# Performance work log

Hardware: AMD Instinct MI355X
Metric: run time of the kernel (lower is better)

The kernel has to match this reference:

```python
import jax, jax.numpy as jnp
import numpy as np

B, C, H, W = 8, 32, 512, 512
WS = 8
CQ = C // 4                      # 8
N = (H // WS) * (W // WS)        # 4096 windows
ED = WS * WS * C                 # 2048 embed_dim
EPS = 1e-6


def setup_inputs() -> dict:
    key = jax.random.key(0)
    ks = jax.random.split(key, 16)
    s = 0.02
    return {
        "input_x": jax.random.normal(ks[0], (B, C, H, W), jnp.float32),
        # in_conv: Conv2d(C, C//4, 1)
        "w_in": jax.random.normal(ks[1], (CQ, C), jnp.float32) * s,
        "b_in": jnp.zeros((CQ,), jnp.float32),
        # conv: Conv2d(C, C//4, 1) + LayerNorm(C//4)
        "w_conv": jax.random.normal(ks[2], (CQ, C), jnp.float32) * s,
        "b_conv": jnp.zeros((CQ,), jnp.float32),
        "ln_w": jnp.ones((CQ,), jnp.float32),
        "ln_b": jnp.zeros((CQ,), jnp.float32),
        # out_CA: Conv2d(C//4, C, 1)
        "w_ca": jax.random.normal(ks[3], (C, CQ), jnp.float32) * s,
        "b_ca": jnp.zeros((C,), jnp.float32),
        # out_SA: Conv2d(C//4, 1, 3, pad 1)
        "w_sa": jax.random.normal(ks[4], (1, CQ, 3, 3), jnp.float32) * s,
        "b_sa": jnp.zeros((1,), jnp.float32),
        # out_mask MLP: Linear(ED, ED//2), Linear(ED//2, ED)  (torch weight [out,in])
        "w_m1": jax.random.normal(ks[5], (ED // 2, ED), jnp.float32) * s,
        "b_m1": jnp.zeros((ED // 2,), jnp.float32),
        "w_m2": jax.random.normal(ks[6], (ED, ED // 2), jnp.float32) * s,
        "b_m2": jnp.zeros((ED,), jnp.float32),
    }


def _leaky(x):
    return jax.nn.leaky_relu(x, 0.1)


def _conv1x1(x, w, b):
    # x: [B,Cin,H,W], w: [Cout,Cin]
    return jnp.einsum('bchw,oc->bohw', x, w) + b[None, :, None, None]


def reference(input_x, w_in, b_in, w_conv, b_conv, ln_w, ln_b,
              w_ca, b_ca, w_sa, b_sa, w_m1, b_m1, w_m2, b_m2):
    b_, c_, h_, w_ = input_x.shape
    n_win = (h_ // WS) * (w_ // WS)

    # in_conv branch
    x = _leaky(_conv1x1(input_x, w_in, b_in))          # [B,CQ,H,W]

    # conv branch: 1x1 conv -> channels_first LayerNorm -> leaky
    x_ = _conv1x1(input_x, w_conv, b_conv)             # [B,CQ,H,W]
    u = jnp.mean(x_, axis=1, keepdims=True)
    s = jnp.mean((x_ - u) ** 2, axis=1, keepdims=True)
    x_ = (x_ - u) / jnp.sqrt(s + EPS)
    x_ = _leaky(ln_w[None, :, None, None] * x_ + ln_b[None, :, None, None])

    # channel attention: global avg pool -> 1x1 conv -> sigmoid
    pooled = jnp.mean(x_, axis=(2, 3), keepdims=True)  # [B,CQ,1,1]
    ca = jax.nn.sigmoid(_conv1x1(pooled, w_ca, b_ca))  # [B,C,1,1]

    # spatial attention: 3x3 conv -> sigmoid
    sa = jax.lax.conv_general_dilated(
        x_, w_sa, (1, 1), 'SAME',
        dimension_numbers=('NCHW', 'OIHW', 'NCHW')) + b_sa[None, :, None, None]
    sa = jax.nn.sigmoid(sa)                            # [B,1,H,W]

    # window variance + bottom-k mask
    xm = jnp.mean(x, axis=1)                           # [B,H,W]
    xw = xm.reshape(b_, h_ // WS, WS, w_ // WS, WS)
    xw = xw.transpose(0, 1, 3, 2, 4).reshape(b_, n_win, WS * WS)  # [B,N,64]
    var_x = jnp.var(xw, axis=-1, ddof=1)               # [B,N] (torch unbiased var)
    k_top = n_win // 2
    _, idx = jax.lax.top_k(-var_x, k_top)              # indices of smallest-variance windows
    mask = jnp.ones((b_, n_win), input_x.dtype)
    mask = mask.at[jnp.arange(b_)[:, None], idx].set(0.0)  # vectorized scatter

    # broadcast 0/1 mask across embed dim, then MLP (see notes re: original bug)
    m = jnp.broadcast_to(mask[:, :, None], (b_, n_win, w_m1.shape[1]))
    hdd = _leaky(jnp.einsum('bnd,ed->bne', m, w_m1) + b_m1)
    out_mask = jnp.einsum('bne,fe->bnf', hdd, w_m2) + b_m2  # [B,N,ED]

    return (out_mask, ca, sa)
```

## Files before the change

kernel.cpp:

```cpp
#include <hip/hip_runtime.h>
#include <math.h>

#define B_   8
#define C_   32
#define H_   512
#define W_   512
#define CQ_  8
#define NW_  4096
#define ED_  2048
#define EH_  1024
#define EPS_ 1e-6f

#define AS1 __attribute__((address_space(1)))
#define AS3 __attribute__((address_space(3)))

__device__ __forceinline__ float leaky(float x) { return x > 0.f ? x : 0.1f * x; }
__device__ __forceinline__ float sigmoidf_(float x) { return 1.f / (1.f + __expf(-x)); }

__global__ __launch_bounds__(256) void pass_a(
    const float* __restrict__ x,
    const float* __restrict__ w_in, const float* __restrict__ b_in,
    const float* __restrict__ w_conv, const float* __restrict__ b_conv,
    const float* __restrict__ ln_w, const float* __restrict__ ln_b,
    float* __restrict__ xq_out,
    double* __restrict__ var_out,
    float* __restrict__ pooled_part)
{
    __shared__ float stage[4][6][256];
    __shared__ float red[4][CQ_];

    const int tid  = threadIdx.x;
    const int lane = tid & 63, wv = tid >> 6;
    const int sx   = blockIdx.x;
    const int band = blockIdx.y;
    const int b    = blockIdx.z;
    const size_t plane = (size_t)H_ * W_;
    const float* xb = x + (size_t)b * C_ * plane;

    const int row0 = band * 8 + (lane >> 3);
    const int col0 = sx * 128 + wv * 32 + (lane & 7) * 4;
    const float* gw = xb + (size_t)row0 * W_ + col0;

#define STAGE(slot, c)                                                         \
    __builtin_amdgcn_global_load_lds(                                          \
        (const AS1 unsigned int*)(gw + (size_t)(c) * plane),                   \
        (AS3 unsigned int*)(&stage[wv][slot][0]), 16, 0, 0);

    float ycv[CQ_][4], yin[CQ_][4];
#pragma unroll
    for (int q = 0; q < CQ_; ++q)
#pragma unroll
        for (int j = 0; j < 4; ++j) { ycv[q][j] = 0.f; yin[q][j] = 0.f; }

    STAGE(0, 0) STAGE(1, 1) STAGE(2, 2) STAGE(3, 3) STAGE(4, 4) STAGE(5, 5)

#pragma unroll
    for (int c = 0; c < C_; ++c) {
        if (c < 27)       asm volatile("s_waitcnt vmcnt(5)" ::: "memory");
        else if (c == 27) asm volatile("s_waitcnt vmcnt(4)" ::: "memory");
        else if (c == 28) asm volatile("s_waitcnt vmcnt(3)" ::: "memory");
        else if (c == 29) asm volatile("s_waitcnt vmcnt(2)" ::: "memory");
        else if (c == 30) asm volatile("s_waitcnt vmcnt(1)" ::: "memory");
        else              asm volatile("s_waitcnt vmcnt(0)" ::: "memory");

        const float4 v = *reinterpret_cast<const float4*>(&stage[wv][c % 6][lane * 4]);
#pragma unroll
        for (int q = 0; q < CQ_; ++q) {
            const float wc = w_conv[q * C_ + c];
            const float wi = w_in[q * C_ + c];
            ycv[q][0] = fmaf(wc, v.x, ycv[q][0]);
            ycv[q][1] = fmaf(wc, v.y, ycv[q][1]);
            ycv[q][2] = fmaf(wc, v.z, ycv[q][2]);
            ycv[q][3] = fmaf(wc, v.w, ycv[q][3]);
            yin[q][0] = fmaf(wi, v.x, yin[q][0]);
            yin[q][1] = fmaf(wi, v.y, yin[q][1]);
            yin[q][2] = fmaf(wi, v.z, yin[q][2]);
            yin[q][3] = fmaf(wi, v.w, yin[q][3]);
        }
        if (c + 6 < C_) {
            asm volatile("s_waitcnt lgkmcnt(0)" ::: "memory");
            STAGE(c % 6, c + 6)
        }
    }
#undef STAGE

#pragma unroll
    for (int q = 0; q < CQ_; ++q) {
        const float bc = b_conv[q];
#pragma unroll
        for (int j = 0; j < 4; ++j) ycv[q][j] += bc;
    }

    float ps[CQ_];
#pragma unroll
    for (int q = 0; q < CQ_; ++q) ps[q] = 0.f;

    float xmv[4];
#pragma unroll
    for (int j = 0; j < 4; ++j) {
        float u = 0.f;
#pragma unroll
        for (int q = 0; q < CQ_; ++q) u += ycv[q][j];
        u *= 0.125f;
        float s = 0.f;
#pragma unroll
        for (int q = 0; q < CQ_; ++q) { const float d = ycv[q][j] - u; s = fmaf(d, d, s); }
        s *= 0.125f;
        const float inv = 1.f / sqrtf(s + EPS_);
        float m = 0.f;
#pragma unroll
        for (int q = 0; q < CQ_; ++q) {
            const float xv = leaky(fmaf(ln_w[q], (ycv[q][j] - u) * inv, ln_b[q]));
            ycv[q][j] = xv;
            ps[q] += xv;
            m += leaky(yin[q][j] + b_in[q]);
        }
        xmv[j] = m * 0.125f;
    }

#pragma unroll
    for (int q = 0; q < CQ_; ++q) {
        *reinterpret_cast<float4*>(
            &xq_out[(((size_t)b * CQ_ + q) * H_ + row0) * W_ + col0]) =
            make_float4(ycv[q][0], ycv[q][1], ycv[q][2], ycv[q][3]);
    }

    {
        double s = (double)xmv[0] + (double)xmv[1] + (double)xmv[2] + (double)xmv[3];
        s += __shfl_xor(s, 1);
        s += __shfl_xor(s, 8);
        s += __shfl_xor(s, 16);
        s += __shfl_xor(s, 32);
        const double mean = s * (1.0 / 64.0);
        double s2 = 0.0;
#pragma unroll
        for (int j = 0; j < 4; ++j) {
            const double d = (double)xmv[j] - mean;
            s2 += d * d;
        }
        s2 += __shfl_xor(s2, 1);
        s2 += __shfl_xor(s2, 8);
        s2 += __shfl_xor(s2, 16);
        s2 += __shfl_xor(s2, 32);
        if ((lane >> 3) == 0 && (lane & 1) == 0) {
            const int k = (lane & 7) >> 1;
            const int n = band * 64 + sx * 16 + wv * 4 + k;
            var_out[(size_t)b * NW_ + n] = s2 * (1.0 / 63.0);
        }
    }

#pragma unroll
    for (int q = 0; q < CQ_; ++q) {
        float s = ps[q];
#pragma unroll
        for (int off = 32; off; off >>= 1) s += __shfl_xor(s, off);
        if (lane == 0) red[wv][q] = s;
    }
    __syncthreads();
    if (tid < CQ_) {
        const float s = red[0][tid] + red[1][tid] + red[2][tid] + red[3][tid];
        const int bid = ((int)blockIdx.z * 64 + blockIdx.y) * 4 + blockIdx.x;
        pooled_part[bid * CQ_ + tid] = s;
    }
}

__global__ __launch_bounds__(256) void sa_kernel(
    const float* __restrict__ xq,
    const float* __restrict__ w_sa, const float* __restrict__ b_sa,
    float* __restrict__ sa_out)
{
    __shared__ float xl[CQ_][18][72];
    const int tid = threadIdx.x;
    const int b = blockIdx.z;
    const int ty = blockIdx.y * 16, tx = blockIdx.x * 64;

    for (int idx = tid; idx < CQ_ * 18 * 18; idx += 256) {
        const int ch = idx / 324;
        const int rem = idx % 324;
        const int r = rem / 18, c4 = rem % 18;
        const int gy = ty + r - 1;
        const int gxf = tx + c4 * 4 - 4;
        float4 v = make_float4(0.f, 0.f, 0.f, 0.f);
        if (gy >= 0 && gy < H_ && gxf >= 0 && gxf < W_)
            v = *reinterpret_cast<const float4*>(
                    &xq[(((size_t)b * CQ_ + ch) * H_ + gy) * W_ + gxf]);
        *reinterpret_cast<float4*>(&xl[ch][r][c4 * 4]) = v;
    }
    __syncthreads();

    const int px = (tid & 15) * 4, py = tid >> 4;
    const float bsa = b_sa[0];
    float acc[4] = {bsa, bsa, bsa, bsa};
#pragma unroll
    for (int q = 0; q < CQ_; ++q) {
#pragma unroll
        for (int dy = 0; dy < 3; ++dy) {
            const float* r = &xl[q][py + dy][px];
            const float4 aa = *reinterpret_cast<const float4*>(r);
            const float4 bb = *reinterpret_cast<const float4*>(r + 4);
            const float4 cc = *reinterpret_cast<const float4*>(r + 8);
            const float a[12] = {aa.x, aa.y, aa.z, aa.w, bb.x, bb.y, bb.z, bb.w,
                                 cc.x, cc.y, cc.z, cc.w};
#pragma unroll
            for (int dx = 0; dx < 3; ++dx) {
                const float w = w_sa[q * 9 + dy * 3 + dx];
#pragma unroll
                for (int j = 0; j < 4; ++j) acc[j] = fmaf(w, a[j + 3 + dx], acc[j]);
            }
        }
    }
    const float4 o = make_float4(sigmoidf_(acc[0]), sigmoidf_(acc[1]),
                                 sigmoidf_(acc[2]), sigmoidf_(acc[3]));
    *reinterpret_cast<float4*>(&sa_out[((size_t)b * H_ + (ty + py)) * W_ + tx + px]) = o;
}

__global__ __launch_bounds__(256) void k2_kernel(
    const double* __restrict__ var, float* __restrict__ maskF,
    const float* __restrict__ w_m1, const float* __restrict__ b_m1,
    float* __restrict__ h1, float* __restrict__ h0,
    const float* __restrict__ pooled_part,
    const float* __restrict__ w_ca, const float* __restrict__ b_ca,
    float* __restrict__ ca_out)
{
    __shared__ double sv[NW_];
    const int bi = blockIdx.x;
    const int tid = threadIdx.x;

    if (bi < 128) {
        const int b = bi >> 4;
        const double* vb = var + (size_t)b * NW_;
        for (int j = tid; j < NW_; j += 256) sv[j] = vb[j];
        __syncthreads();
        const int i = (bi & 15) * 256 + tid;
        const double vi = sv[i];
        int cnt = 0;
#pragma unroll 4
        for (int j = 0; j < NW_; ++j) {
            const double vj = sv[j];
            cnt += (vj < vi) || (vj == vi && j < i);
        }
        maskF[(size_t)b * NW_ + i] = (cnt < NW_ / 2) ? 0.f : 1.f;
    } else if (bi < 384) {
        const int wave = tid >> 6, lane = tid & 63;
        const int e = (bi - 128) * 4 + wave;
        const float* row = w_m1 + (size_t)e * ED_;
        float s = 0.f;
#pragma unroll
        for (int k = 0; k < ED_ / 64; ++k) s += row[lane + 64 * k];
#pragma unroll
        for (int off = 32; off; off >>= 1) s += __shfl_xor(s, off);
        if (lane == 0) {
            h1[e] = leaky(s + b_m1[e]);
            h0[e] = leaky(b_m1[e]);
        }
    } else {
        float* sp = (float*)sv;
        const int bq = tid >> 2, part = tid & 3;
        const int bb = bq >> 3, q = bq & 7;
        float s = 0.f;
        for (int k = part; k < 256; k += 4)
            s += pooled_part[((size_t)bb * 256 + k) * CQ_ + q];
        sp[tid] = s;
        __syncthreads();
        if (tid < 64)
            sp[256 + tid] = (sp[4 * tid] + sp[4 * tid + 1] + sp[4 * tid + 2] + sp[4 * tid + 3])
                            * (1.f / ((float)H_ * (float)W_));
        __syncthreads();
        const int ob = tid >> 5, o = tid & 31;
        float acc = b_ca[o];
#pragma unroll
        for (int qq = 0; qq < CQ_; ++qq)
            acc = fmaf(w_ca[o * CQ_ + qq], sp[256 + ob * CQ_ + qq], acc);
        ca_out[tid] = sigmoidf_(acc);
    }
}

__global__ __launch_bounds__(256) void o_kernel(const float* __restrict__ w_m2,
                                                const float* __restrict__ b_m2,
                                                const float* __restrict__ h1,
                                                const float* __restrict__ h0,
                                                float* __restrict__ o1, float* __restrict__ o0)
{
    const int wave = threadIdx.x >> 6, lane = threadIdx.x & 63;
    const int f = blockIdx.x * 4 + wave;
    const float* row = w_m2 + (size_t)f * EH_;
    float s1 = 0.f, s0 = 0.f;
#pragma unroll
    for (int k = 0; k < EH_ / 64; ++k) {
        const float w = row[lane + 64 * k];
        s1 = fmaf(w, h1[lane + 64 * k], s1);
        s0 = fmaf(w, h0[lane + 64 * k], s0);
    }
#pragma unroll
    for (int off = 32; off; off >>= 1) {
        s1 += __shfl_xor(s1, off);
        s0 += __shfl_xor(s0, off);
    }
    if (lane == 0) {
        o1[f] = s1 + b_m2[f];
        o0[f] = s0 + b_m2[f];
    }
}

__global__ __launch_bounds__(256) void bcast_kernel(const float* __restrict__ maskF,
                                                    const float* __restrict__ o1,
                                                    const float* __restrict__ o0,
                                                    float* __restrict__ out)
{
    __shared__ float sm[16];
    const int t = threadIdx.x;
    const long row0 = (long)blockIdx.x * 16;
    if (t < 16) sm[t] = maskF[row0 + t];
    const float4 a1 = ((const float4*)o1)[t], b1 = ((const float4*)o1)[t + 256];
    const float4 a0 = ((const float4*)o0)[t], b0 = ((const float4*)o0)[t + 256];
    __syncthreads();
#pragma unroll
    for (int r = 0; r < 16; ++r) {
        float4* dst = (float4*)(out + (size_t)(row0 + r) * ED_);
        const bool m = sm[r] > 0.5f;
        dst[t]       = m ? a1 : a0;
        dst[t + 256] = m ? b1 : b0;
    }
}

extern "C" void kernel_launch(void* const* d_in, const int* in_sizes, int n_in,
                              void* d_out, int out_size, void* d_ws, size_t ws_size,
                              hipStream_t stream)
{
    const float* x    = (const float*)d_in[0];
    const float* w_in = (const float*)d_in[1];
    const float* b_in = (const float*)d_in[2];
    const float* w_cv = (const float*)d_in[3];
    const float* b_cv = (const float*)d_in[4];
    const float* lnw  = (const float*)d_in[5];
    const float* lnb  = (const float*)d_in[6];
    const float* w_ca = (const float*)d_in[7];
    const float* b_ca = (const float*)d_in[8];
    const float* w_sa = (const float*)d_in[9];
    const float* b_sa = (const float*)d_in[10];
    const float* w_m1 = (const float*)d_in[11];
    const float* b_m1 = (const float*)d_in[12];
    const float* w_m2 = (const float*)d_in[13];
    const float* b_m2 = (const float*)d_in[14];

    float* out_mask = (float*)d_out;
    float* ca_out   = out_mask + (size_t)B_ * NW_ * ED_;
    float* sa_out   = ca_out + (size_t)B_ * C_;

    float* xq = out_mask;

    char* ws = (char*)d_ws;
    double* var       = (double*)ws;
    float*  maskF     = (float*)(ws + (size_t)B_ * NW_ * 8);
    float*  pooled_pp = maskF + (size_t)B_ * NW_;
    float*  h1 = pooled_pp + 2048 * CQ_;
    float*  h0 = h1 + EH_;
    float*  o1 = h0 + EH_;
    float*  o0 = o1 + ED_;

    pass_a<<<dim3(4, 64, B_), 256, 0, stream>>>(
        x, w_in, b_in, w_cv, b_cv, lnw, lnb, xq, var, pooled_pp);
    sa_kernel<<<dim3(8, 32, B_), 256, 0, stream>>>(xq, w_sa, b_sa, sa_out);
    k2_kernel<<<385, 256, 0, stream>>>(var, maskF, w_m1, b_m1, h1, h0,
                                       pooled_pp, w_ca, b_ca, ca_out);
    o_kernel<<<ED_ / 4, 256, 0, stream>>>(w_m2, b_m2, h1, h0, o1, o0);
    bcast_kernel<<<B_ * NW_ / 16, 256, 0, stream>>>(maskF, o1, o0, out_mask);
}
```

Baseline: 324.9 us.

## Replace LDS-staged async loads with register double-buffered float4 loads in pass_a

The 1x1-conv input pass now loads channel planes straight into registers as float4, with two 8-channel register buffers (16 loads in flight), instead of staging through LDS with global_load_lds and manual vmcnt waits. This removes the LDS round-trip and the per-channel lgkmcnt stalls. The launch bounds also request 2 blocks per SM, which caps register use. The extra 32 live float4 registers on top of 64 accumulators could cause spilling or lower occupancy.

Measured after the change: 329.1 us. No clear change (+1.3%).

```diff
diff --git a/kernel.cpp b/kernel.cpp
--- a/kernel.cpp
+++ b/kernel.cpp
@@ -11,13 +11,10 @@
 #define EH_  1024
 #define EPS_ 1e-6f
 
-#define AS1 __attribute__((address_space(1)))
-#define AS3 __attribute__((address_space(3)))
-
 __device__ __forceinline__ float leaky(float x) { return x > 0.f ? x : 0.1f * x; }
 __device__ __forceinline__ float sigmoidf_(float x) { return 1.f / (1.f + __expf(-x)); }
 
-__global__ __launch_bounds__(256) void pass_a(
+__global__ __launch_bounds__(256, 2) void pass_a(
     const float* __restrict__ x,
     const float* __restrict__ w_in, const float* __restrict__ b_in,
     const float* __restrict__ w_conv, const float* __restrict__ b_conv,
@@ -26,7 +23,6 @@
     double* __restrict__ var_out,
     float* __restrict__ pooled_part)
 {
-    __shared__ float stage[4][6][256];
     __shared__ float red[4][CQ_];
 
     const int tid  = threadIdx.x;
@@ -39,12 +35,7 @@
 
     const int row0 = band * 8 + (lane >> 3);
     const int col0 = sx * 128 + wv * 32 + (lane & 7) * 4;
-    const float* gw = xb + (size_t)row0 * W_ + col0;
-
-#define STAGE(slot, c)                                                         \
-    __builtin_amdgcn_global_load_lds(                                          \
-        (const AS1 unsigned int*)(gw + (size_t)(c) * plane),                   \
-        (AS3 unsigned int*)(&stage[wv][slot][0]), 16, 0, 0);
+    const float* gp = xb + (size_t)row0 * W_ + col0;
 
     float ycv[CQ_][4], yin[CQ_][4];
 #pragma unroll
@@ -52,37 +43,52 @@
 #pragma unroll
         for (int j = 0; j < 4; ++j) { ycv[q][j] = 0.f; yin[q][j] = 0.f; }
 
-    STAGE(0, 0) STAGE(1, 1) STAGE(2, 2) STAGE(3, 3) STAGE(4, 4) STAGE(5, 5)
-
-#pragma unroll
-    for (int c = 0; c < C_; ++c) {
-        if (c < 27)       asm volatile("s_waitcnt vmcnt(5)" ::: "memory");
-        else if (c == 27) asm volatile("s_waitcnt vmcnt(4)" ::: "memory");
-        else if (c == 28) asm volatile("s_waitcnt vmcnt(3)" ::: "memory");
-        else if (c == 29) asm volatile("s_waitcnt vmcnt(2)" ::: "memory");
-        else if (c == 30) asm volatile("s_waitcnt vmcnt(1)" ::: "memory");
-        else              asm volatile("s_waitcnt vmcnt(0)" ::: "memory");
-
-        const float4 v = *reinterpret_cast<const float4*>(&stage[wv][c % 6][lane * 4]);
-#pragma unroll
-        for (int q = 0; q < CQ_; ++q) {
-            const float wc = w_conv[q * C_ + c];
-            const float wi = w_in[q * C_ + c];
-            ycv[q][0] = fmaf(wc, v.x, ycv[q][0]);
-            ycv[q][1] = fmaf(wc, v.y, ycv[q][1]);
-            ycv[q][2] = fmaf(wc, v.z, ycv[q][2]);
-            ycv[q][3] = fmaf(wc, v.w, ycv[q][3]);
-            yin[q][0] = fmaf(wi, v.x, yin[q][0]);
-            yin[q][1] = fmaf(wi, v.y, yin[q][1]);
-            yin[q][2] = fmaf(wi, v.z, yin[q][2]);
-            yin[q][3] = fmaf(wi, v.w, yin[q][3]);
-        }
-        if (c + 6 < C_) {
-            asm volatile("s_waitcnt lgkmcnt(0)" ::: "memory");
-            STAGE(c % 6, c + 6)
-        }
-    }
-#undef STAGE
+#define LD(c) (*reinterpret_cast<const float4*>(gp + (size_t)(c) * plane))
+#define FMA1(c, v)                                                     \
+    {                                                                  \
+        _Pragma("unroll")                                              \
+        for (int q = 0; q < CQ_; ++q) {                                \
+            const float wc = w_conv[q * C_ + (c)];                     \
+            const float wi = w_in[q * C_ + (c)];                       \
+            ycv[q][0] = fmaf(wc, (v).x, ycv[q][0]);                    \
+            ycv[q][1] = fmaf(wc, (v).y, ycv[q][1]);                    \
+            ycv[q][2] = fmaf(wc, (v).z, ycv[q][2]);                    \
+            ycv[q][3] = fmaf(wc, (v).w, ycv[q][3]);                    \
+            yin[q][0] = fmaf(wi, (v).x, yin[q][0]);                    \
+            yin[q][1] = fmaf(wi, (v).y, yin[q][1]);                    \
+            yin[q][2] = fmaf(wi, (v).z, yin[q][2]);                    \
+            yin[q][3] = fmaf(wi, (v).w, yin[q][3]);                    \
+        }                                                              \
+    }
+
+    float4 a0, a1, a2, a3, a4, a5, a6, a7;
+    float4 b0, b1, b2, b3, b4, b5, b6, b7;
+
+    a0 = LD(0);  a1 = LD(1);  a2 = LD(2);  a3 = LD(3);
+    a4 = LD(4);  a5 = LD(5);  a6 = LD(6);  a7 = LD(7);
+    b0 = LD(8);  b1 = LD(9);  b2 = LD(10); b3 = LD(11);
+    b4 = LD(12); b5 = LD(13); b6 = LD(14); b7 = LD(15);
+
+    FMA1(0, a0) FMA1(1, a1) FMA1(2, a2) FMA1(3, a3)
+    FMA1(4, a4) FMA1(5, a5) FMA1(6, a6) FMA1(7, a7)
+
+    a0 = LD(16); a1 = LD(17); a2 = LD(18); a3 = LD(19);
+    a4 = LD(20); a5 = LD(21); a6 = LD(22); a7 = LD(23);
+
+    FMA1(8, b0)  FMA1(9, b1)  FMA1(10, b2) FMA1(11, b3)
+    FMA1(12, b4) FMA1(13, b5) FMA1(14, b6) FMA1(15, b7)
+
+    b0 = LD(24); b1 = LD(25); b2 = LD(26); b3 = LD(27);
+    b4 = LD(28); b5 = LD(29); b6 = LD(30); b7 = LD(31);
+
+    FMA1(16, a0) FMA1(17, a1) FMA1(18, a2) FMA1(19, a3)
+    FMA1(20, a4) FMA1(21, a5) FMA1(22, a6) FMA1(23, a7)
+
+    FMA1(24, b0) FMA1(25, b1) FMA1(26, b2) FMA1(27, b3)
+    FMA1(28, b4) FMA1(29, b5) FMA1(30, b6) FMA1(31, b7)
+
+#undef LD
+#undef FMA1
 
 #pragma unroll
     for (int q = 0; q < CQ_; ++q) {
```
